# Kernel optimization log

Hardware: AMD Instinct MI355X
Metric: run time of the kernel (lower is better)

The kernel has to match this reference:

```python
import jax, jax.numpy as jnp
import numpy as np

B, S, D = 8, 512, 768
H, C = 256, 32


def setup_inputs() -> dict:
    key = jax.random.key(0)
    ks = jax.random.split(key, 8)
    scale = 0.05
    return {
        "seq_feats": jax.random.normal(ks[0], (B, S, D), jnp.float32),
        "U": jax.random.normal(ks[1], (H, C, H), jnp.float32) * scale,
        "W_w": jax.random.normal(ks[2], (C, 2 * H), jnp.float32) * scale,
        "W_b": jax.random.normal(ks[3], (C,), jnp.float32) * scale,
        "Ws_w": jax.random.normal(ks[4], (H, D), jnp.float32) * scale,
        "Ws_b": jax.random.normal(ks[5], (H,), jnp.float32) * scale,
        "We_w": jax.random.normal(ks[6], (H, D), jnp.float32) * scale,
        "We_b": jax.random.normal(ks[7], (H,), jnp.float32) * scale,
    }


def reference(seq_feats, U, W_w, W_b, Ws_w, Ws_b, We_w, We_b):
    # start / end projections (torch Linear: x @ W.T + b)
    Hs = seq_feats @ Ws_w.T + Ws_b  # [B,S,H]
    He = seq_feats @ We_w.T + We_b  # [B,S,H]
    # bilinear term: h_s^T U h_e per label
    biaff = jnp.einsum('bsh,hcg,beg->bsec', Hs, U, He)  # [B,S,S,C]
    # concat-linear term rewritten as two broadcast matmuls:
    # W([Hs;He]) = Hs @ W_s.T + He @ W_e.T + b  (identical math, no [B,S,S,2H] intermediate)
    h = Hs.shape[-1]
    W_s, W_e = W_w[:, :h], W_w[:, h:]
    lin = (Hs @ W_s.T)[:, :, None, :] + (He @ W_e.T)[:, None, :, :] + W_b
    return biaff + lin
```

## Files before the change

kernel.cpp:

```cpp
#include <hip/hip_runtime.h>


typedef __bf16 bf16x8 __attribute__((ext_vector_type(8)));
typedef float f32x4 __attribute__((ext_vector_type(4)));

union BF8 { unsigned short s[8]; unsigned int u[4]; bf16x8 v; };

__device__ __forceinline__ unsigned short f2bf(float f) {
    unsigned u = __builtin_bit_cast(unsigned, f);
    u += 0x7fffu + ((u >> 16) & 1u);
    return (unsigned short)(u >> 16);
}
__device__ __forceinline__ float bf2f(unsigned short s) {
    unsigned u = ((unsigned)s) << 16;
    return __builtin_bit_cast(float, u);
}
__device__ __forceinline__ bf16x8 load_bf8(const unsigned short* p) {
    return __builtin_bit_cast(bf16x8, *reinterpret_cast<const uint4*>(p));
}
__device__ __forceinline__ ushort4 pack4(float4 v) {
    ushort4 r;
    r.x = f2bf(v.x); r.y = f2bf(v.y); r.z = f2bf(v.z); r.w = f2bf(v.w);
    return r;
}

__global__ __launch_bounds__(256) void kp_conv(
    const float* __restrict__ seq, const float* __restrict__ Ws_w,
    const float* __restrict__ We_w, unsigned short* __restrict__ seqb,
    unsigned short* __restrict__ Wcat) {
    int i = blockIdx.x * 256 + threadIdx.x;
    if (i < 786432) {
        float4 v = ((const float4*)seq)[i];
        ((ushort4*)seqb)[i] = pack4(v);
    } else {
        int j = i - 786432;
        float4 v = (j < 49152) ? ((const float4*)Ws_w)[j]
                               : ((const float4*)We_w)[j - 49152];
        ((ushort4*)Wcat)[j] = pack4(v);
    }
}

__global__ __launch_bounds__(256) void k0_ut(const float* __restrict__ U,
                                             unsigned short* __restrict__ Ut) {
    __shared__ float tile[32][33];
    int tx = threadIdx.x, ty = threadIdx.y;
    int J0 = blockIdx.x * 32, h0 = blockIdx.y * 32;
#pragma unroll
    for (int i = 0; i < 4; i++)
        tile[ty + 8 * i][tx] = U[(h0 + ty + 8 * i) * 8192 + J0 + tx];
    __syncthreads();
#pragma unroll
    for (int i = 0; i < 4; i++)
        Ut[(J0 + ty + 8 * i) * 256 + h0 + tx] = f2bf(tile[tx][ty + 8 * i]);
}

__global__ __launch_bounds__(256) void k1_hs_he(
    const unsigned short* __restrict__ seqb, const unsigned short* __restrict__ Wcat,
    const float* __restrict__ Ws_b, const float* __restrict__ We_b,
    unsigned short* __restrict__ Hs, unsigned short* __restrict__ He) {
    int wid = threadIdx.x >> 6, lane = threadIdx.x & 63;
    int t = lane & 15, q = lane >> 4;
    int wave_id = blockIdx.x * 4 + wid;
    int m0 = (wave_id >> 4) * 32;
    int n0 = (wave_id & 15) * 32;

    const unsigned short* a0 = seqb + (size_t)(m0 + t) * 768;
    const unsigned short* a1 = seqb + (size_t)(m0 + 16 + t) * 768;
    const unsigned short* b0 = Wcat + (size_t)(n0 + t) * 768;
    const unsigned short* b1 = Wcat + (size_t)(n0 + 16 + t) * 768;

    f32x4 acc[2][2];
#pragma unroll
    for (int i = 0; i < 2; i++)
#pragma unroll
        for (int j = 0; j < 2; j++) acc[i][j] = {0.f, 0.f, 0.f, 0.f};

#pragma unroll 4
    for (int kk = 0; kk < 24; kk++) {
        int k = kk * 32 + q * 8;
        bf16x8 af0 = load_bf8(a0 + k);
        bf16x8 af1 = load_bf8(a1 + k);
        bf16x8 bf0 = load_bf8(b0 + k);
        bf16x8 bf1 = load_bf8(b1 + k);
        acc[0][0] = __builtin_amdgcn_mfma_f32_16x16x32_bf16(af0, bf0, acc[0][0], 0, 0, 0);
        acc[0][1] = __builtin_amdgcn_mfma_f32_16x16x32_bf16(af0, bf1, acc[0][1], 0, 0, 0);
        acc[1][0] = __builtin_amdgcn_mfma_f32_16x16x32_bf16(af1, bf0, acc[1][0], 0, 0, 0);
        acc[1][1] = __builtin_amdgcn_mfma_f32_16x16x32_bf16(af1, bf1, acc[1][1], 0, 0, 0);
    }
#pragma unroll
    for (int nt = 0; nt < 2; nt++) {
        int col = n0 + nt * 16 + t;
        float bv;
        unsigned short* dst;
        int c2;
        if (col < 256) { bv = Ws_b[col]; dst = Hs; c2 = col; }
        else           { bv = We_b[col - 256]; dst = He; c2 = col - 256; }
#pragma unroll
        for (int mt = 0; mt < 2; mt++)
#pragma unroll
            for (int r = 0; r < 4; r++) {
                int row = m0 + mt * 16 + q * 4 + r;
                dst[row * 256 + c2] = f2bf(acc[mt][nt][r] + bv);
            }
    }
}

__global__ __launch_bounds__(256) void k2_lin(
    const unsigned short* __restrict__ Hs, const unsigned short* __restrict__ He,
    const float* __restrict__ W_w, const float* __restrict__ W_b,
    float* __restrict__ linS, float* __restrict__ linE) {
    int idx = blockIdx.x * 256 + threadIdx.x;
    int c = idx & 31;
    int rowid = idx >> 5;
    int which = rowid >> 12;
    int bs = rowid & 4095;
    const unsigned short* Hrow = (which ? He : Hs) + bs * 256;
    const float* Wrow = W_w + c * 512 + which * 256;
    float acc = which ? W_b[c] : 0.f;
#pragma unroll 4
    for (int h8 = 0; h8 < 32; h8++) {
        BF8 hv;
        hv.v = load_bf8(Hrow + h8 * 8);
        float4 w0 = *(const float4*)(Wrow + h8 * 8);
        float4 w1 = *(const float4*)(Wrow + h8 * 8 + 4);
        acc += bf2f(hv.s[0]) * w0.x + bf2f(hv.s[1]) * w0.y + bf2f(hv.s[2]) * w0.z +
               bf2f(hv.s[3]) * w0.w + bf2f(hv.s[4]) * w1.x + bf2f(hv.s[5]) * w1.y +
               bf2f(hv.s[6]) * w1.z + bf2f(hv.s[7]) * w1.w;
    }
    (which ? linE : linS)[bs * 32 + c] = acc;
}

__global__ __launch_bounds__(256) void k3_T(
    const unsigned short* __restrict__ Hs, const unsigned short* __restrict__ Ut,
    unsigned short* __restrict__ T) {
    int wid = threadIdx.x >> 6, lane = threadIdx.x & 63;
    int t = lane & 15, q = lane >> 4;
    int n_blk = blockIdx.x & 63;
    int mb = (blockIdx.x >> 6) * 4 + wid;
    int c = n_blk >> 1;
    int g0 = (n_blk & 1) * 128;
    int s0 = mb * 32;

    bf16x8 afr[2][8];
#pragma unroll
    for (int mt = 0; mt < 2; mt++) {
        const unsigned short* arow = Hs + (s0 + mt * 16 + t) * 256 + q * 8;
#pragma unroll
        for (int kk = 0; kk < 8; kk++) afr[mt][kk] = load_bf8(arow + kk * 32);
    }
#pragma unroll 2
    for (int nt = 0; nt < 8; nt++) {
        const unsigned short* brow = Ut + (size_t)(c * 256 + g0 + nt * 16 + t) * 256 + q * 8;
        f32x4 acc0 = {0.f, 0.f, 0.f, 0.f}, acc1 = {0.f, 0.f, 0.f, 0.f};
#pragma unroll
        for (int kk = 0; kk < 8; kk++) {
            bf16x8 b = load_bf8(brow + kk * 32);
            acc0 = __builtin_amdgcn_mfma_f32_16x16x32_bf16(afr[0][kk], b, acc0, 0, 0, 0);
            acc1 = __builtin_amdgcn_mfma_f32_16x16x32_bf16(afr[1][kk], b, acc1, 0, 0, 0);
        }
        int g = g0 + nt * 16 + t;
#pragma unroll
        for (int r = 0; r < 4; r++) {
            int s_a = s0 + q * 4 + r;
            int s_b = s_a + 16;
            T[(size_t)(s_a * 32 + c) * 256 + g] = f2bf(acc0[r]);
            T[(size_t)(s_b * 32 + c) * 256 + g] = f2bf(acc1[r]);
        }
    }
}

__global__ __launch_bounds__(256) void k4_out(
    const unsigned short* __restrict__ T, const unsigned short* __restrict__ He,
    const float* __restrict__ linS, const float* __restrict__ linE,
    float* __restrict__ out) {
    int wid = threadIdx.x >> 6, lane = threadIdx.x & 63;
    int t = lane & 15, q = lane >> 4;
    int b = blockIdx.x & 7;
    int s = (blockIdx.x >> 3) * 4 + wid;
    int bs = b * 512 + s;

    bf16x8 bfr[2][8];
#pragma unroll
    for (int nt = 0; nt < 2; nt++) {
        const unsigned short* brow = T + (size_t)(bs * 32 + nt * 16 + t) * 256 + q * 8;
#pragma unroll
        for (int kk = 0; kk < 8; kk++) bfr[nt][kk] = load_bf8(brow + kk * 32);
    }
    float ls0 = linS[bs * 32 + t];
    float ls1 = linS[bs * 32 + 16 + t];
    float* orow = out + (size_t)bs * (512 * 32);
#pragma unroll 2
    for (int e_t = 0; e_t < 32; e_t++) {
        int e0 = e_t * 16;
        const unsigned short* arow = He + (size_t)(b * 512 + e0 + t) * 256 + q * 8;
        f32x4 acc0 = {0.f, 0.f, 0.f, 0.f}, acc1 = {0.f, 0.f, 0.f, 0.f};
#pragma unroll
        for (int kk = 0; kk < 8; kk++) {
            bf16x8 a = load_bf8(arow + kk * 32);
            acc0 = __builtin_amdgcn_mfma_f32_16x16x32_bf16(a, bfr[0][kk], acc0, 0, 0, 0);
            acc1 = __builtin_amdgcn_mfma_f32_16x16x32_bf16(a, bfr[1][kk], acc1, 0, 0, 0);
        }
#pragma unroll
        for (int r = 0; r < 4; r++) {
            int e = e0 + q * 4 + r;
            float le0 = linE[(b * 512 + e) * 32 + t];
            float le1 = linE[(b * 512 + e) * 32 + 16 + t];
            orow[e * 32 + t] = acc0[r] + ls0 + le0;
            orow[e * 32 + 16 + t] = acc1[r] + ls1 + le1;
        }
    }
}

extern "C" void kernel_launch(void* const* d_in, const int* in_sizes, int n_in,
                              void* d_out, int out_size, void* d_ws, size_t ws_size,
                              hipStream_t stream) {
    const float* seq  = (const float*)d_in[0];
    const float* U    = (const float*)d_in[1];
    const float* W_w  = (const float*)d_in[2];
    const float* W_b  = (const float*)d_in[3];
    const float* Ws_w = (const float*)d_in[4];
    const float* Ws_b = (const float*)d_in[5];
    const float* We_w = (const float*)d_in[6];
    const float* We_b = (const float*)d_in[7];
    float* out = (float*)d_out;

    char* ws = (char*)d_ws;
    unsigned short* Hs   = (unsigned short*)(ws);
    unsigned short* He   = (unsigned short*)(ws + (2ull << 20));
    unsigned short* Ut   = (unsigned short*)(ws + (4ull << 20));
    float* linS          = (float*)(ws + (8ull << 20));
    float* linE          = (float*)(ws + (8ull << 20) + (1ull << 19));
    unsigned short* seqb = (unsigned short*)(ws + (9ull << 20));
    unsigned short* Wcat = (unsigned short*)(ws + (15ull << 20));
    unsigned short* T    = (unsigned short*)(ws + (16ull << 20));

    kp_conv<<<3456, 256, 0, stream>>>(seq, Ws_w, We_w, seqb, Wcat);
    k0_ut<<<dim3(256, 8), dim3(32, 8), 0, stream>>>(U, Ut);
    k1_hs_he<<<512, 256, 0, stream>>>(seqb, Wcat, Ws_b, We_b, Hs, He);
    k2_lin<<<1024, 256, 0, stream>>>(Hs, He, W_w, W_b, linS, linE);
    k3_T<<<2048, 256, 0, stream>>>(Hs, Ut, T);
    k4_out<<<1024, 256, 0, stream>>>(T, He, linS, linE, out);
}
```

Baseline: 542.5 us.

## Fold end-linear term into bilinear GEMM and vectorize output stores

Initializes the Hs·U accumulator with the W_e weight row, so the subsequent product with He yields the He·W_e term for free. This removes the linE buffer and half of the linear kernel. MFMA operand order is swapped in both GEMM kernels so each lane owns contiguous columns, which allows packed bf16 stores for T and 16-byte fp32 nontemporal stores for the output. The start-linear term is preloaded as the accumulator. Folding W_e into bf16-rounded T slightly changes rounding.

```diff
diff --git a/kernel.cpp b/kernel.cpp
--- a/kernel.cpp
+++ b/kernel.cpp
@@ -3,6 +3,8 @@
 
 typedef __bf16 bf16x8 __attribute__((ext_vector_type(8)));
 typedef float f32x4 __attribute__((ext_vector_type(4)));
+typedef unsigned int u32x4 __attribute__((ext_vector_type(4)));
+typedef unsigned int u32x2 __attribute__((ext_vector_type(2)));
 
 union BF8 { unsigned short s[8]; unsigned int u[4]; bf16x8 v; };
 
@@ -106,17 +108,14 @@
 }
 
 __global__ __launch_bounds__(256) void k2_lin(
-    const unsigned short* __restrict__ Hs, const unsigned short* __restrict__ He,
-    const float* __restrict__ W_w, const float* __restrict__ W_b,
-    float* __restrict__ linS, float* __restrict__ linE) {
+    const unsigned short* __restrict__ Hs, const float* __restrict__ W_w,
+    const float* __restrict__ W_b, float* __restrict__ linS) {
     int idx = blockIdx.x * 256 + threadIdx.x;
     int c = idx & 31;
-    int rowid = idx >> 5;
-    int which = rowid >> 12;
-    int bs = rowid & 4095;
-    const unsigned short* Hrow = (which ? He : Hs) + bs * 256;
-    const float* Wrow = W_w + c * 512 + which * 256;
-    float acc = which ? W_b[c] : 0.f;
+    int bs = idx >> 5;
+    const unsigned short* Hrow = Hs + bs * 256;
+    const float* Wrow = W_w + c * 512;
+    float acc = W_b[c];
 #pragma unroll 4
     for (int h8 = 0; h8 < 32; h8++) {
         BF8 hv;
@@ -127,12 +126,12 @@
                bf2f(hv.s[3]) * w0.w + bf2f(hv.s[4]) * w1.x + bf2f(hv.s[5]) * w1.y +
                bf2f(hv.s[6]) * w1.z + bf2f(hv.s[7]) * w1.w;
     }
-    (which ? linE : linS)[bs * 32 + c] = acc;
+    linS[bs * 32 + c] = acc;
 }
 
 __global__ __launch_bounds__(256) void k3_T(
     const unsigned short* __restrict__ Hs, const unsigned short* __restrict__ Ut,
-    unsigned short* __restrict__ T) {
+    const float* __restrict__ W_w, unsigned short* __restrict__ T) {
     int wid = threadIdx.x >> 6, lane = threadIdx.x & 63;
     int t = lane & 15, q = lane >> 4;
     int n_blk = blockIdx.x & 63;
@@ -141,73 +140,77 @@
     int g0 = (n_blk & 1) * 128;
     int s0 = mb * 32;
 
-    bf16x8 afr[2][8];
+    bf16x8 hfr[2][8];
 #pragma unroll
     for (int mt = 0; mt < 2; mt++) {
-        const unsigned short* arow = Hs + (s0 + mt * 16 + t) * 256 + q * 8;
-#pragma unroll
-        for (int kk = 0; kk < 8; kk++) afr[mt][kk] = load_bf8(arow + kk * 32);
+        const unsigned short* arow = Hs + (size_t)(s0 + mt * 16 + t) * 256 + q * 8;
+#pragma unroll
+        for (int kk = 0; kk < 8; kk++) hfr[mt][kk] = load_bf8(arow + kk * 32);
     }
 #pragma unroll 2
     for (int nt = 0; nt < 8; nt++) {
-        const unsigned short* brow = Ut + (size_t)(c * 256 + g0 + nt * 16 + t) * 256 + q * 8;
-        f32x4 acc0 = {0.f, 0.f, 0.f, 0.f}, acc1 = {0.f, 0.f, 0.f, 0.f};
+        const unsigned short* grow = Ut + (size_t)(c * 256 + g0 + nt * 16 + t) * 256 + q * 8;
+        float4 we = *(const float4*)(W_w + c * 512 + 256 + g0 + nt * 16 + q * 4);
+        f32x4 acc0 = {we.x, we.y, we.z, we.w};
+        f32x4 acc1 = acc0;
 #pragma unroll
         for (int kk = 0; kk < 8; kk++) {
-            bf16x8 b = load_bf8(brow + kk * 32);
-            acc0 = __builtin_amdgcn_mfma_f32_16x16x32_bf16(afr[0][kk], b, acc0, 0, 0, 0);
-            acc1 = __builtin_amdgcn_mfma_f32_16x16x32_bf16(afr[1][kk], b, acc1, 0, 0, 0);
+            bf16x8 g = load_bf8(grow + kk * 32);
+            acc0 = __builtin_amdgcn_mfma_f32_16x16x32_bf16(g, hfr[0][kk], acc0, 0, 0, 0);
+            acc1 = __builtin_amdgcn_mfma_f32_16x16x32_bf16(g, hfr[1][kk], acc1, 0, 0, 0);
         }
-        int g = g0 + nt * 16 + t;
-#pragma unroll
-        for (int r = 0; r < 4; r++) {
-            int s_a = s0 + q * 4 + r;
-            int s_b = s_a + 16;
-            T[(size_t)(s_a * 32 + c) * 256 + g] = f2bf(acc0[r]);
-            T[(size_t)(s_b * 32 + c) * 256 + g] = f2bf(acc1[r]);
-        }
+        int gidx = g0 + nt * 16 + q * 4;
+        u32x2 p0, p1;
+        p0.x = (unsigned)f2bf(acc0[0]) | ((unsigned)f2bf(acc0[1]) << 16);
+        p0.y = (unsigned)f2bf(acc0[2]) | ((unsigned)f2bf(acc0[3]) << 16);
+        p1.x = (unsigned)f2bf(acc1[0]) | ((unsigned)f2bf(acc1[1]) << 16);
+        p1.y = (unsigned)f2bf(acc1[2]) | ((unsigned)f2bf(acc1[3]) << 16);
+        __builtin_nontemporal_store(p0, (u32x2*)(T + (size_t)((s0 + t) * 32 + c) * 256 + gidx));
+        __builtin_nontemporal_store(p1, (u32x2*)(T + (size_t)((s0 + 16 + t) * 32 + c) * 256 + gidx));
     }
 }
 
 __global__ __launch_bounds__(256) void k4_out(
     const unsigned short* __restrict__ T, const unsigned short* __restrict__ He,
-    const float* __restrict__ linS, const float* __restrict__ linE,
-    float* __restrict__ out) {
+    const float* __restrict__ linS, float* __restrict__ out) {
     int wid = threadIdx.x >> 6, lane = threadIdx.x & 63;
     int t = lane & 15, q = lane >> 4;
     int b = blockIdx.x & 7;
     int s = (blockIdx.x >> 3) * 4 + wid;
     int bs = b * 512 + s;
 
-    bf16x8 bfr[2][8];
-#pragma unroll
-    for (int nt = 0; nt < 2; nt++) {
-        const unsigned short* brow = T + (size_t)(bs * 32 + nt * 16 + t) * 256 + q * 8;
-#pragma unroll
-        for (int kk = 0; kk < 8; kk++) bfr[nt][kk] = load_bf8(brow + kk * 32);
-    }
-    float ls0 = linS[bs * 32 + t];
-    float ls1 = linS[bs * 32 + 16 + t];
+    bf16x8 tfr[2][8];
+#pragma unroll
+    for (int ct = 0; ct < 2; ct++) {
+        const unsigned short* brow = T + (size_t)(bs * 32 + ct * 16 + t) * 256 + q * 8;
+#pragma unroll
+        for (int kk = 0; kk < 8; kk++) {
+            u32x4 r = __builtin_nontemporal_load((const u32x4*)(brow + kk * 32));
+            tfr[ct][kk] = __builtin_bit_cast(bf16x8, r);
+        }
+    }
+    f32x4 ls0, ls1;
+    {
+        float4 a = *(const float4*)(linS + bs * 32 + q * 4);
+        float4 bv = *(const float4*)(linS + bs * 32 + 16 + q * 4);
+        ls0 = {a.x, a.y, a.z, a.w};
+        ls1 = {bv.x, bv.y, bv.z, bv.w};
+    }
     float* orow = out + (size_t)bs * (512 * 32);
 #pragma unroll 2
     for (int e_t = 0; e_t < 32; e_t++) {
         int e0 = e_t * 16;
         const unsigned short* arow = He + (size_t)(b * 512 + e0 + t) * 256 + q * 8;
-        f32x4 acc0 = {0.f, 0.f, 0.f, 0.f}, acc1 = {0.f, 0.f, 0.f, 0.f};
+        f32x4 acc0 = ls0, acc1 = ls1;
 #pragma unroll
         for (int kk = 0; kk < 8; kk++) {
             bf16x8 a = load_bf8(arow + kk * 32);
-            acc0 = __builtin_amdgcn_mfma_f32_16x16x32_bf16(a, bfr[0][kk], acc0, 0, 0, 0);
-            acc1 = __builtin_amdgcn_mfma_f32_16x16x32_bf16(a, bfr[1][kk], acc1, 0, 0, 0);
+            acc0 = __builtin_amdgcn_mfma_f32_16x16x32_bf16(tfr[0][kk], a, acc0, 0, 0, 0);
+            acc1 = __builtin_amdgcn_mfma_f32_16x16x32_bf16(tfr[1][kk], a, acc1, 0, 0, 0);
         }
-#pragma unroll
-        for (int r = 0; r < 4; r++) {
-            int e = e0 + q * 4 + r;
-            float le0 = linE[(b * 512 + e) * 32 + t];
-            float le1 = linE[(b * 512 + e) * 32 + 16 + t];
-            orow[e * 32 + t] = acc0[r] + ls0 + le0;
-            orow[e * 32 + 16 + t] = acc1[r] + ls1 + le1;
-        }
+        float* p = orow + (size_t)(e0 + t) * 32 + q * 4;
+        __builtin_nontemporal_store(acc0, (f32x4*)p);
+        __builtin_nontemporal_store(acc1, (f32x4*)(p + 16));
     }
 }
 
@@ -229,7 +232,6 @@
     unsigned short* He   = (unsigned short*)(ws + (2ull << 20));
     unsigned short* Ut   = (unsigned short*)(ws + (4ull << 20));
     float* linS          = (float*)(ws + (8ull << 20));
-    float* linE          = (float*)(ws + (8ull << 20) + (1ull << 19));
     unsigned short* seqb = (unsigned short*)(ws + (9ull << 20));
     unsigned short* Wcat = (unsigned short*)(ws + (15ull << 20));
     unsigned short* T    = (unsigned short*)(ws + (16ull << 20));
@@ -237,7 +239,7 @@
     kp_conv<<<3456, 256, 0, stream>>>(seq, Ws_w, We_w, seqb, Wcat);
     k0_ut<<<dim3(256, 8), dim3(32, 8), 0, stream>>>(U, Ut);
     k1_hs_he<<<512, 256, 0, stream>>>(seqb, Wcat, Ws_b, We_b, Hs, He);
-    k2_lin<<<1024, 256, 0, stream>>>(Hs, He, W_w, W_b, linS, linE);
-    k3_T<<<2048, 256, 0, stream>>>(Hs, Ut, T);
-    k4_out<<<1024, 256, 0, stream>>>(T, He, linS, linE, out);
-}
+    k2_lin<<<512, 256, 0, stream>>>(Hs, W_w, W_b, linS);
+    k3_T<<<2048, 256, 0, stream>>>(Hs, Ut, W_w, T);
+    k4_out<<<1024, 256, 0, stream>>>(T, He, linS, out);
+}
```

Result: faster. 509.2 us (-6.1%).
